# Kernel tuning notes

Hardware: AMD Instinct MI355X
Metric: run time of the kernel (lower is better)

The kernel has to match this reference:

```python
import jax, jax.numpy as jnp
import numpy as np

FRACTAL_OUTPUT = (5, 5)            # (a, b); requires 5 * num_kernels == a*b
PERC_THRESHOLD = 0.59275
NEXT_SHAPE = (224, 224)
K_END = int(0.4 * FRACTAL_OUTPUT[0] * FRACTAL_OUTPUT[1] + 1)   # 11
KERNEL_SIZES = list(range(3, K_END + 1, 2))                    # [3,5,7,9,11]


def setup_inputs() -> dict:
    key = jax.random.key(0)
    inputs = jax.random.uniform(key, (64, 224, 224, 3), dtype=jnp.float32) * 255.0
    return {"inputs": inputs}


def _extract_patches(x, k):
    # tf.image.extract_patches(sizes=strides=k, SAME) == zero-pad + space-to-depth
    B, H, W, C = x.shape
    rows, cols = -(-H // k), -(-W // k)
    ph, pw = rows * k - H, cols * k - W
    x = jnp.pad(x, ((0, 0), (ph // 2, ph - ph // 2), (pw // 2, pw - pw // 2), (0, 0)))
    x = x.reshape(B, rows, k, cols, k, C).transpose(0, 1, 3, 2, 4, 5)
    return x.reshape(B * rows * cols, k, k, C), rows * cols


def _binarize(patches, k, ch):
    # distance function: 1 iff |channel value - center pixel channel value| <= k
    center = patches[:, k // 2, k // 2, ch][:, None, None]
    return (jnp.abs(patches[..., ch] - center) <= k).astype(jnp.int32)


def _connected_stats(binp, k):
    # 4-connected components via min-label propagation (== tfa connected_components
    # up to relabeling; we only need #components and max label count incl. background)
    N = binp.shape[0]
    idx = jnp.arange(1, k * k + 1, dtype=jnp.int32).reshape(k, k)
    INF = jnp.int32(k * k + 2)
    lbl0 = jnp.where(binp > 0, idx, 0)

    def step(_, lbl):
        v = jnp.where(binp > 0, lbl, INF)
        pad = lambda a, w: jnp.pad(a, ((0, 0),) + w, constant_values=INF)
        up    = pad(v, ((1, 0), (0, 0)))[:, :-1, :]
        down  = pad(v, ((0, 1), (0, 0)))[:, 1:, :]
        left  = pad(v, ((0, 0), (1, 0)))[:, :, :-1]
        right = pad(v, ((0, 0), (0, 1)))[:, :, 1:]
        m = jnp.minimum(jnp.minimum(v, up), jnp.minimum(jnp.minimum(down, left), right))
        return jnp.where(binp > 0, m, 0)

    lbl = jax.lax.fori_loop(0, k * k, step, lbl0)  # k*k iters guarantee convergence
    ncomp = jnp.sum((binp > 0) & (lbl == idx), axis=(1, 2)).astype(jnp.int32)
    lblf = lbl.reshape(N, k * k)
    cnt = jnp.zeros((N, k * k + 1), jnp.int32).at[jnp.arange(N)[:, None], lblf].add(1)
    return ncomp, cnt.max(axis=1)  # (#components, most-common label count incl bg 0)


def _components(inputs, k, ch):
    B = inputs.shape[0]
    patches, P = _extract_patches(inputs, k)
    binp = _binarize(patches, k, ch)                    # (B*P, k, k)
    ones = binp.sum(axis=(1, 2)).reshape(B, P)          # int counts per patch
    # tf.bincount(minlength=1, maxlength=k*k): bins 0..k*k-1, value k*k dropped
    cnt = jnp.zeros((B, k * k + 1), jnp.float32).at[jnp.arange(B)[:, None], ones].add(1.0)
    prob = cnt[:, : k * k] / P                          # (B, k*k)
    n = jnp.arange(1, k * k + 1, dtype=jnp.float32)
    fd = (prob / n).sum(1)
    m = (prob * n).sum(1)
    m2 = ((prob * prob) * n).sum(1)
    lac = (m2 - m * m) / (m * m)
    perc = ((ones.astype(jnp.float32) / (k * k)) >= PERC_THRESHOLD).astype(jnp.int32)
    acp = perc.sum(1) // P                              # tf integer reduce_mean
    ncomp, marea = _connected_stats(binp, k)
    acn = ncomp.reshape(B, P).sum(1) // P
    acma = marea.reshape(B, P).sum(1) // P
    return jnp.stack([acn.astype(jnp.float32), acp.astype(jnp.float32),
                      acma.astype(jnp.float32), lac, fd], axis=1)   # (B, 5)


def _rearrange(c):
    # group metric-major: all acn over kernels, then acp, acma, lac, fd
    return jnp.concatenate([c[:, mm::5] for mm in range(5)], axis=1)


def reference(inputs):
    B = inputs.shape[0]
    chans = []
    for ch in range(3):
        comps = jnp.concatenate([_components(inputs, k, ch) for k in KERNEL_SIZES], axis=1)
        chans.append(_rearrange(comps).reshape(B, FRACTAL_OUTPUT[0], FRACTAL_OUTPUT[1]))
    out = jnp.stack(chans, axis=3)                      # (B, a, b, 3)
    return jax.image.resize(out, (B, NEXT_SHAPE[0], NEXT_SHAPE[1], 3), method='bilinear')
```

## Files before the change

kernel.cpp:

```cpp
#include <hip/hip_runtime.h>

#define HW 224
#define NIMG 64
#define NPIX ((size_t)NIMG * HW * HW)
#define NSLICE 8
#define ACC_STRIDE 128
#define NCOMBO (NIMG * 15)
#define ACC_BYTES (NCOMBO * ACC_STRIDE * 4)

typedef unsigned long long u64;

struct U128 { u64 lo, hi; };

__device__ __forceinline__ u64  u_or  (u64 a, u64 b){ return a | b; }
__device__ __forceinline__ u64  u_and (u64 a, u64 b){ return a & b; }
__device__ __forceinline__ u64  u_andn(u64 a, u64 b){ return a & ~b; }
__device__ __forceinline__ bool u_eq(u64 a, u64 b){ return a == b; }
__device__ __forceinline__ bool u_nz(u64 a){ return a != 0ull; }
__device__ __forceinline__ u64  u_shl(u64 a, int n){ return a << n; }
__device__ __forceinline__ u64  u_shr(u64 a, int n){ return a >> n; }
__device__ __forceinline__ int  u_pop(u64 a){ return __popcll(a); }
__device__ __forceinline__ u64  u_low(u64 a){ return a & (0ull - a); }

__device__ __forceinline__ U128 u_or  (U128 a, U128 b){ return {a.lo|b.lo, a.hi|b.hi}; }
__device__ __forceinline__ U128 u_and (U128 a, U128 b){ return {a.lo&b.lo, a.hi&b.hi}; }
__device__ __forceinline__ U128 u_andn(U128 a, U128 b){ return {a.lo&~b.lo, a.hi&~b.hi}; }
__device__ __forceinline__ bool u_eq(U128 a, U128 b){ return a.lo==b.lo && a.hi==b.hi; }
__device__ __forceinline__ bool u_nz(U128 a){ return (a.lo | a.hi) != 0ull; }
__device__ __forceinline__ U128 u_shl(U128 a, int n){
    return { a.lo << n, (a.hi << n) | (a.lo >> (64 - n)) };
}
__device__ __forceinline__ U128 u_shr(U128 a, int n){
    return { (a.lo >> n) | (a.hi << (64 - n)), a.hi >> n };
}
__device__ __forceinline__ int u_pop(U128 a){ return __popcll(a.lo) + __popcll(a.hi); }
__device__ __forceinline__ U128 u_low(U128 a){
    if (a.lo) return { a.lo & (0ull - a.lo), 0ull };
    return { 0ull, a.hi & (0ull - a.hi) };
}

template<bool B, class T, class F> struct sel        { using type = T; };
template<class T, class F>         struct sel<false, T, F> { using type = F; };

template<int K>
__device__ __forceinline__ void load_row(const float* __restrict__ p, float* r) {
#pragma unroll
    for (int j = 0; j + 4 <= K; j += 4) {
        float4 v; __builtin_memcpy(&v, p + j, 16);
        r[j] = v.x; r[j + 1] = v.y; r[j + 2] = v.z; r[j + 3] = v.w;
    }
    if constexpr ((K & 3) >= 2) {
        constexpr int b = (K / 4) * 4;
        float2 v; __builtin_memcpy(&v, p + b, 8);
        r[b] = v.x; r[b + 1] = v.y;
    }
    if constexpr (K & 1) r[K - 1] = p[K - 1];
}

template<int K, int S, class M>
__device__ __forceinline__ void do_patch(const float* __restrict__ img, int p,
                                         M leftCol, M rightCol,
                                         int* bins, int& t_perc, int& t_ncomp,
                                         int& t_marea) {
    constexpr int KK   = K * K;
    constexpr int ROWS = (HW + K - 1) / K;
    constexpr int PAD  = (ROWS * K - HW) / 2;

    const int pr = p / ROWS, pc = p - pr * ROWS;
    const int y0 = pr * K - PAD, x0 = pc * K - PAD;

    M msk;
    if constexpr (KK <= 64) msk = 0ull; else msk = U128{0, 0};

    const bool fast = (S == 1) && (y0 >= 0) && (x0 >= 0) &&
                      (y0 + K <= HW) && (x0 + K <= HW);
    if (fast) {
        if constexpr (K <= 9) {
            float r[K][K];
#pragma unroll
            for (int i = 0; i < K; i++)
                load_row<K>(img + (size_t)(y0 + i) * HW + x0, r[i]);
            const float cen = r[K / 2][K / 2];
#pragma unroll
            for (int i = 0; i < K; i++) {
#pragma unroll
                for (int j = 0; j < K; j++) {
                    const u64 bit = (fabsf(r[i][j] - cen) <= (float)K) ? 1ull : 0ull;
                    const int cb = i * K + j;
                    if constexpr (KK <= 64) msk |= bit << cb;
                    else { if (cb < 64) msk.lo |= bit << cb; else msk.hi |= bit << (cb - 64); }
                }
            }
        } else {
            const float cen = img[(size_t)(y0 + K / 2) * HW + (x0 + K / 2)];
#pragma unroll
            for (int i = 0; i < K; i++) {
                float r[K];
                load_row<K>(img + (size_t)(y0 + i) * HW + x0, r);
#pragma unroll
                for (int j = 0; j < K; j++) {
                    const u64 bit = (fabsf(r[j] - cen) <= (float)K) ? 1ull : 0ull;
                    const int cb = i * K + j;
                    if constexpr (KK <= 64) msk |= bit << cb;
                    else { if (cb < 64) msk.lo |= bit << cb; else msk.hi |= bit << (cb - 64); }
                }
            }
        }
    } else {
        const float cen = img[((size_t)(y0 + K / 2) * HW + (x0 + K / 2)) * S];
#pragma unroll
        for (int i = 0; i < K; i++) {
            const int y = y0 + i;
            const bool yin = (unsigned)y < (unsigned)HW;
#pragma unroll
            for (int j = 0; j < K; j++) {
                const int x = x0 + j;
                const bool inb = yin && ((unsigned)x < (unsigned)HW);
                const float v = inb ? img[((size_t)y * HW + x) * S] : 0.0f;
                const u64 bit = (fabsf(v - cen) <= (float)K) ? 1ull : 0ull;
                const int cb = i * K + j;
                if constexpr (KK <= 64) msk |= bit << cb;
                else { if (cb < 64) msk.lo |= bit << cb; else msk.hi |= bit << (cb - 64); }
            }
        }
    }
    const int ones = u_pop(msk);

    M nbm = u_or(u_or(u_shl(u_andn(msk, rightCol), 1),
                      u_shr(u_andn(msk, leftCol ), 1)),
                 u_or(u_shl(msk, K), u_shr(msk, K)));
    M iso = u_andn(msk, nbm);
    const int niso = u_pop(iso);
    int ncomp = niso, maxsz = (niso > 0) ? 1 : 0;
    M m = u_andn(msk, iso);
    while (u_nz(m)) {
        M s = u_low(m);
        for (;;) {
            M g = u_or(s, u_or(u_or(u_shl(u_andn(s, rightCol), 1),
                                    u_shr(u_andn(s, leftCol ), 1)),
                               u_or(u_shl(s, K), u_shr(s, K))));
            g = u_and(g, m);
            if (u_eq(g, s)) break;
            s = g;
        }
        ncomp++;
        const int sz = u_pop(s);
        if (sz > maxsz) maxsz = sz;
        m = u_andn(m, s);
    }

    const int bgcnt = KK - ones;
    const int marea = (bgcnt > maxsz) ? bgcnt : maxsz;
    t_ncomp += ncomp;
    t_marea += marea;
    if ((float)ones / (float)KK >= 0.59275f) t_perc++;
    atomicAdd(&bins[ones], 1);
}

template<int K>
__device__ __forceinline__ void make_colmasks(u64& lcl, u64& lch, u64& rcl, u64& rch) {
    lcl = lch = rcl = rch = 0;
#pragma unroll
    for (int i = 0; i < K; i++) {
        const int cl = i * K, cr = i * K + K - 1;
        if (cl < 64) lcl |= 1ull << cl; else lch |= 1ull << (cl - 64);
        if (cr < 64) rcl |= 1ull << cr; else rch |= 1ull << (cr - 64);
    }
}

template<int K, int S>
__device__ __forceinline__ void job_body(const float* __restrict__ img,
                                         int slice, int lane, int* hist,
                                         int* __restrict__ gout) {
    constexpr int ROWS = (HW + K - 1) / K;
    constexpr int P    = ROWS * ROWS;
    constexpr int KK   = K * K;
    using M = typename sel<(KK <= 64), u64, U128>::type;

    u64 lcl, lch, rcl, rch;
    make_colmasks<K>(lcl, lch, rcl, rch);
    M leftCol, rightCol;
    if constexpr (KK <= 64) { leftCol = lcl; rightCol = rcl; }
    else { leftCol = U128{lcl, lch}; rightCol = U128{rcl, rch}; }

    for (int s = lane; s <= KK; s += 64) hist[s] = 0;

    const int pstart = (slice * P) / NSLICE;
    const int pend   = ((slice + 1) * P) / NSLICE;

    int t_perc = 0, t_ncomp = 0, t_marea = 0;
    if constexpr (K <= 5) {
#pragma unroll 2
        for (int p = pstart + lane; p < pend; p += 64)
            do_patch<K, S, M>(img, p, leftCol, rightCol, hist,
                              t_perc, t_ncomp, t_marea);
    } else {
        for (int p = pstart + lane; p < pend; p += 64)
            do_patch<K, S, M>(img, p, leftCol, rightCol, hist,
                              t_perc, t_ncomp, t_marea);
    }

#pragma unroll
    for (int off = 32; off; off >>= 1) {
        t_perc  += __shfl_down(t_perc,  off);
        t_ncomp += __shfl_down(t_ncomp, off);
        t_marea += __shfl_down(t_marea, off);
    }
    if (lane == 0) {
        atomicAdd(&gout[124], t_perc);
        atomicAdd(&gout[125], t_ncomp);
        atomicAdd(&gout[126], t_marea);
    }
    for (int s = lane; s <= KK; s += 64) {
        const int v = hist[s];
        if (v) atomicAdd(&gout[s], v);
    }
}

template<int S>
__global__ __launch_bounds__(64) void fractal_stats(const float* __restrict__ in,
                                                    int* __restrict__ gacc) {
    const int B     = blockIdx.x;
    const int x     = B & 7;
    const int j     = B >> 3;
    const int gl    = j / 40;
    const int inner = j - gl * 40;
    const int g     = gl * 8 + x;
    const int b     = g / 3, ch = g - b * 3;
    const int kidx  = inner >> 3;
    const int slice = inner & 7;

    __shared__ int hist[124];

    const float* img = (S == 1) ? in + ((size_t)ch * NIMG + b) * HW * HW
                                : in + (size_t)b * HW * HW * 3 + ch;
    int* gout = gacc + (g * 5 + kidx) * ACC_STRIDE;

    switch (kidx) {
        case 0: job_body<3,  S>(img, slice, threadIdx.x, hist, gout); break;
        case 1: job_body<5,  S>(img, slice, threadIdx.x, hist, gout); break;
        case 2: job_body<7,  S>(img, slice, threadIdx.x, hist, gout); break;
        case 3: job_body<9,  S>(img, slice, threadIdx.x, hist, gout); break;
        case 4: job_body<11, S>(img, slice, threadIdx.x, hist, gout); break;
    }
}

__global__ __launch_bounds__(256) void fractal_resize_acc(const int* __restrict__ gacc,
                                                          float* __restrict__ out,
                                                          int total) {
    const int q = blockIdx.x, b = blockIdx.y;
    __shared__ float vals[75];

    if (threadIdx.x < 15) {
        const int rem  = threadIdx.x;
        const int ch   = rem / 5;
        const int kidx = rem % 5;
        const int K    = 3 + 2 * kidx;
        const int ROWS = (HW + K - 1) / K;
        const int P    = ROWS * ROWS;
        const int KK   = K * K;

        const int* a = gacc + (b * 15 + rem) * ACC_STRIDE;
        const float Pf = (float)P;
        float fd = 0.0f, m1 = 0.0f, m2 = 0.0f;
        for (int s = 0; s < KK; s++) {
            const float prob = (float)a[s] / Pf;
            const float n = (float)(s + 1);
            fd += prob / n;
            m1 += prob * n;
            m2 += prob * prob * n;
        }
        const float lac = (m2 - m1 * m1) / (m1 * m1);
        vals[(0 * 5 + kidx) * 3 + ch] = (float)(a[125] / P);
        vals[(1 * 5 + kidx) * 3 + ch] = (float)(a[124] / P);
        vals[(2 * 5 + kidx) * 3 + ch] = (float)(a[126] / P);
        vals[(3 * 5 + kidx) * 3 + ch] = lac;
        vals[(4 * 5 + kidx) * 3 + ch] = fd;
    }
    __syncthreads();

    const int x = threadIdx.x;
    if (x >= HW) return;

    const float sc = 5.0f / 224.0f;
    const float ux = ((float)x + 0.5f) * sc - 0.5f;
    const float fx = floorf(ux);
    const float wx = ux - fx;
    int x0 = (int)fx, x1 = x0 + 1;
    if (x0 < 0) x0 = 0; if (x1 > 4) x1 = 4;

    for (int y = q * 56; y < q * 56 + 56; ++y) {
        const float uy = ((float)y + 0.5f) * sc - 0.5f;
        const float fy = floorf(uy);
        const float wy = uy - fy;
        int y0 = (int)fy, y1 = y0 + 1;
        if (y0 < 0) y0 = 0; if (y1 > 4) y1 = 4;

        const float w00 = (1.0f - wy) * (1.0f - wx), w01 = (1.0f - wy) * wx;
        const float w10 = wy * (1.0f - wx),          w11 = wy * wx;

        const int base = ((b * HW + y) * HW + x) * 3;
        if (base + 3 > total) continue;
#pragma unroll
        for (int ch = 0; ch < 3; ch++) {
            out[base + ch] = w00 * vals[(y0 * 5 + x0) * 3 + ch]
                           + w01 * vals[(y0 * 5 + x1) * 3 + ch]
                           + w10 * vals[(y1 * 5 + x0) * 3 + ch]
                           + w11 * vals[(y1 * 5 + x1) * 3 + ch];
        }
    }
}

template<int K, int S>
__device__ __forceinline__ void stats_body_full(const float* __restrict__ img,
                                                float* __restrict__ o,
                                                int hist4[4][124], int* sums) {
    constexpr int KK   = K * K;
    constexpr int ROWS = (HW + K - 1) / K;
    constexpr int P    = ROWS * ROWS;
    using M = typename sel<(KK <= 64), u64, U128>::type;
    const int wid = threadIdx.x >> 6;

    u64 lcl, lch, rcl, rch;
    make_colmasks<K>(lcl, lch, rcl, rch);
    M leftCol, rightCol;
    if constexpr (KK <= 64) { leftCol = lcl; rightCol = rcl; }
    else { leftCol = U128{lcl, lch}; rightCol = U128{rcl, rch}; }

    int t_perc = 0, t_ncomp = 0, t_marea = 0;
    for (int p = threadIdx.x; p < P; p += 256)
        do_patch<K, S, M>(img, p, leftCol, rightCol, hist4[wid],
                          t_perc, t_ncomp, t_marea);

    atomicAdd(&sums[0], t_perc);
    atomicAdd(&sums[1], t_ncomp);
    atomicAdd(&sums[2], t_marea);
    __syncthreads();

    if (threadIdx.x == 0) {
        const float Pf = (float)P;
        float fd = 0.0f, m1 = 0.0f, m2 = 0.0f;
        for (int s = 0; s < KK; s++) {
            const float prob = (float)(hist4[0][s] + hist4[1][s] + hist4[2][s] + hist4[3][s]) / Pf;
            const float n = (float)(s + 1);
            fd += prob / n;
            m1 += prob * n;
            m2 += prob * prob * n;
        }
        const float lac = (m2 - m1 * m1) / (m1 * m1);
        o[0]  = (float)(sums[1] / P);
        o[15] = (float)(sums[0] / P);
        o[30] = (float)(sums[2] / P);
        o[45] = lac;
        o[60] = fd;
    }
}

template<int S>
__global__ __launch_bounds__(256) void fractal_stats_full(const float* __restrict__ in,
                                                          float* __restrict__ interm) {
    const int b    = blockIdx.x / 15;
    const int rem  = blockIdx.x % 15;
    const int ch   = rem / 5;
    const int kidx = rem % 5;

    __shared__ int hist[4][124];
    __shared__ int sums[3];
    for (int i = threadIdx.x; i < 4 * 124; i += 256) ((int*)hist)[i] = 0;
    if (threadIdx.x < 3) sums[threadIdx.x] = 0;
    __syncthreads();

    const float* img = in + (size_t)b * HW * HW * 3 + ch;
    float* o = interm + (size_t)b * 75 + kidx * 3 + ch;

    switch (kidx) {
        case 0: stats_body_full<3,  S>(img, o, hist, sums); break;
        case 1: stats_body_full<5,  S>(img, o, hist, sums); break;
        case 2: stats_body_full<7,  S>(img, o, hist, sums); break;
        case 3: stats_body_full<9,  S>(img, o, hist, sums); break;
        case 4: stats_body_full<11, S>(img, o, hist, sums); break;
    }
}

__global__ __launch_bounds__(256) void fractal_resize(const float* __restrict__ interm,
                                                      float* __restrict__ out, int total) {
    const int x = threadIdx.x;
    if (x >= HW) return;
    const int y = blockIdx.x, b = blockIdx.y;

    const float sc = 5.0f / 224.0f;
    const float uy = ((float)y + 0.5f) * sc - 0.5f;
    const float ux = ((float)x + 0.5f) * sc - 0.5f;

    const float fy = floorf(uy), fx = floorf(ux);
    const float wy = uy - fy,    wx = ux - fx;
    int y0 = (int)fy, x0 = (int)fx;
    int y1 = y0 + 1,  x1 = x0 + 1;
    if (y0 < 0) y0 = 0; if (x0 < 0) x0 = 0;
    if (y1 > 4) y1 = 4; if (x1 > 4) x1 = 4;

    const float w00 = (1.0f - wy) * (1.0f - wx), w01 = (1.0f - wy) * wx;
    const float w10 = wy * (1.0f - wx),          w11 = wy * wx;

    const float* gp = interm + (size_t)b * 75;
    const int base = ((b * HW + y) * HW + x) * 3;
    if (base + 3 > total) return;
#pragma unroll
    for (int ch = 0; ch < 3; ch++) {
        out[base + ch] = w00 * gp[(y0 * 5 + x0) * 3 + ch]
                       + w01 * gp[(y0 * 5 + x1) * 3 + ch]
                       + w10 * gp[(y1 * 5 + x0) * 3 + ch]
                       + w11 * gp[(y1 * 5 + x1) * 3 + ch];
    }
}

__global__ __launch_bounds__(256) void deinterleave(const float* __restrict__ in,
                                                    float* __restrict__ planes,
                                                    int* __restrict__ gacc) {
    const int t = blockIdx.x * 256 + threadIdx.x;
    if (t < ACC_BYTES / 16) {
        const int4 z = make_int4(0, 0, 0, 0);
        ((int4*)gacc)[t] = z;
    }
    const size_t pix = (size_t)t * 4;
    if (pix >= NPIX) return;
    float4 a, b, c;
    __builtin_memcpy(&a, in + pix * 3,     16);
    __builtin_memcpy(&b, in + pix * 3 + 4, 16);
    __builtin_memcpy(&c, in + pix * 3 + 8, 16);
    const float4 p0 = make_float4(a.x, a.w, b.z, c.y);
    const float4 p1 = make_float4(a.y, b.x, b.w, c.z);
    const float4 p2 = make_float4(a.z, b.y, c.x, c.w);
    __builtin_memcpy(planes + pix,            &p0, 16);
    __builtin_memcpy(planes + NPIX + pix,     &p1, 16);
    __builtin_memcpy(planes + 2 * NPIX + pix, &p2, 16);
}

extern "C" void kernel_launch(void* const* d_in, const int* in_sizes, int n_in,
                              void* d_out, int out_size, void* d_ws, size_t ws_size,
                              hipStream_t stream) {
    const float* in = (const float*)d_in[0];
    float* out = (float*)d_out;
    float* interm = (float*)d_ws;

    const size_t acc_off    = 19456;
    const size_t planes_off = acc_off + ACC_BYTES;
    const size_t need = planes_off + 3 * NPIX * sizeof(float);

    if (ws_size >= need) {
        int*   gacc   = (int*)((char*)d_ws + acc_off);
        float* planes = (float*)((char*)d_ws + planes_off);
        deinterleave<<<(int)(NPIX / 4 / 256), 256, 0, stream>>>(in, planes, gacc);
        fractal_stats<1><<<192 * 40, 64, 0, stream>>>(planes, gacc);
        fractal_resize_acc<<<dim3(4, NIMG), 256, 0, stream>>>(gacc, out, out_size);
    } else {
        fractal_stats_full<3><<<NIMG * 15, 256, 0, stream>>>(in, interm);
        fractal_resize<<<dim3(HW, NIMG), 256, 0, stream>>>(interm, out, out_size);
    }
}
```

Baseline: 150.8 us.

## Process all three channels per patch from interleaved input, drop deinterleave pass

Removes the separate deinterleave kernel that wrote three channel planes, and instead has each thread read interleaved RGB rows directly and build three binary masks per patch. The per-patch position math and loads are shared across channels. Work is also rebalanced with per-kernel-size slice counts, 109 blocks per image, and the accumulator is zeroed with a memset. In exchange each thread holds more registers and does three connected-component passes, which may lower occupancy and increase divergence.

```diff
diff --git a/kernel.cpp b/kernel.cpp
--- a/kernel.cpp
+++ b/kernel.cpp
@@ -3,7 +3,6 @@
 #define HW 224
 #define NIMG 64
 #define NPIX ((size_t)NIMG * HW * HW)
-#define NSLICE 8
 #define ACC_STRIDE 128
 #define NCOMBO (NIMG * 15)
 #define ACC_BYTES (NCOMBO * ACC_STRIDE * 4)
@@ -39,91 +38,45 @@
     return { 0ull, a.hi & (0ull - a.hi) };
 }
 
+__device__ __forceinline__ void setbit(u64& m, int cb, u64 bit){ m |= bit << cb; }
+__device__ __forceinline__ void setbit(U128& m, int cb, u64 bit){
+    if (cb < 64) m.lo |= bit << cb; else m.hi |= bit << (cb - 64);
+}
+
 template<bool B, class T, class F> struct sel        { using type = T; };
 template<class T, class F>         struct sel<false, T, F> { using type = F; };
 
-template<int K>
-__device__ __forceinline__ void load_row(const float* __restrict__ p, float* r) {
-#pragma unroll
-    for (int j = 0; j + 4 <= K; j += 4) {
+template<int N>
+__device__ __forceinline__ void load_rowN(const float* __restrict__ p, float* r) {
+#pragma unroll
+    for (int j = 0; j + 4 <= N; j += 4) {
         float4 v; __builtin_memcpy(&v, p + j, 16);
         r[j] = v.x; r[j + 1] = v.y; r[j + 2] = v.z; r[j + 3] = v.w;
     }
-    if constexpr ((K & 3) >= 2) {
-        constexpr int b = (K / 4) * 4;
+    if constexpr ((N & 3) >= 2) {
+        constexpr int b = (N / 4) * 4;
         float2 v; __builtin_memcpy(&v, p + b, 8);
         r[b] = v.x; r[b + 1] = v.y;
     }
-    if constexpr (K & 1) r[K - 1] = p[K - 1];
-}
-
-template<int K, int S, class M>
-__device__ __forceinline__ void do_patch(const float* __restrict__ img, int p,
-                                         M leftCol, M rightCol,
-                                         int* bins, int& t_perc, int& t_ncomp,
-                                         int& t_marea) {
-    constexpr int KK   = K * K;
-    constexpr int ROWS = (HW + K - 1) / K;
-    constexpr int PAD  = (ROWS * K - HW) / 2;
-
-    const int pr = p / ROWS, pc = p - pr * ROWS;
-    const int y0 = pr * K - PAD, x0 = pc * K - PAD;
-
-    M msk;
-    if constexpr (KK <= 64) msk = 0ull; else msk = U128{0, 0};
-
-    const bool fast = (S == 1) && (y0 >= 0) && (x0 >= 0) &&
-                      (y0 + K <= HW) && (x0 + K <= HW);
-    if (fast) {
-        if constexpr (K <= 9) {
-            float r[K][K];
-#pragma unroll
-            for (int i = 0; i < K; i++)
-                load_row<K>(img + (size_t)(y0 + i) * HW + x0, r[i]);
-            const float cen = r[K / 2][K / 2];
-#pragma unroll
-            for (int i = 0; i < K; i++) {
-#pragma unroll
-                for (int j = 0; j < K; j++) {
-                    const u64 bit = (fabsf(r[i][j] - cen) <= (float)K) ? 1ull : 0ull;
-                    const int cb = i * K + j;
-                    if constexpr (KK <= 64) msk |= bit << cb;
-                    else { if (cb < 64) msk.lo |= bit << cb; else msk.hi |= bit << (cb - 64); }
-                }
-            }
-        } else {
-            const float cen = img[(size_t)(y0 + K / 2) * HW + (x0 + K / 2)];
-#pragma unroll
-            for (int i = 0; i < K; i++) {
-                float r[K];
-                load_row<K>(img + (size_t)(y0 + i) * HW + x0, r);
-#pragma unroll
-                for (int j = 0; j < K; j++) {
-                    const u64 bit = (fabsf(r[j] - cen) <= (float)K) ? 1ull : 0ull;
-                    const int cb = i * K + j;
-                    if constexpr (KK <= 64) msk |= bit << cb;
-                    else { if (cb < 64) msk.lo |= bit << cb; else msk.hi |= bit << (cb - 64); }
-                }
-            }
-        }
-    } else {
-        const float cen = img[((size_t)(y0 + K / 2) * HW + (x0 + K / 2)) * S];
-#pragma unroll
-        for (int i = 0; i < K; i++) {
-            const int y = y0 + i;
-            const bool yin = (unsigned)y < (unsigned)HW;
-#pragma unroll
-            for (int j = 0; j < K; j++) {
-                const int x = x0 + j;
-                const bool inb = yin && ((unsigned)x < (unsigned)HW);
-                const float v = inb ? img[((size_t)y * HW + x) * S] : 0.0f;
-                const u64 bit = (fabsf(v - cen) <= (float)K) ? 1ull : 0ull;
-                const int cb = i * K + j;
-                if constexpr (KK <= 64) msk |= bit << cb;
-                else { if (cb < 64) msk.lo |= bit << cb; else msk.hi |= bit << (cb - 64); }
-            }
-        }
-    }
+    if constexpr (N & 1) r[N - 1] = p[N - 1];
+}
+
+template<int K>
+__device__ __forceinline__ void make_colmasks(u64& lcl, u64& lch, u64& rcl, u64& rch) {
+    lcl = lch = rcl = rch = 0;
+#pragma unroll
+    for (int i = 0; i < K; i++) {
+        const int cl = i * K, cr = i * K + K - 1;
+        if (cl < 64) lcl |= 1ull << cl; else lch |= 1ull << (cl - 64);
+        if (cr < 64) rcl |= 1ull << cr; else rch |= 1ull << (cr - 64);
+    }
+}
+
+template<int K, class M>
+__device__ __forceinline__ void finish_mask(M msk, M leftCol, M rightCol,
+                                            int* hist, int& t_perc,
+                                            int& t_ncomp, int& t_marea) {
+    constexpr int KK = K * K;
     const int ones = u_pop(msk);
 
     M nbm = u_or(u_or(u_shl(u_andn(msk, rightCol), 1),
@@ -154,27 +107,97 @@
     t_ncomp += ncomp;
     t_marea += marea;
     if ((float)ones / (float)KK >= 0.59275f) t_perc++;
-    atomicAdd(&bins[ones], 1);
+    atomicAdd(&hist[ones], 1);
+}
+
+template<int K, class M>
+__device__ __forceinline__ void do_patch3(const float* __restrict__ img3, int p,
+                                          M leftCol, M rightCol,
+                                          int hist[3][124],
+                                          int* tp, int* tn, int* tm) {
+    constexpr int ROWS = (HW + K - 1) / K;
+    constexpr int PAD  = (ROWS * K - HW) / 2;
+
+    const int pr = p / ROWS, pc = p - pr * ROWS;
+    const int y0 = pr * K - PAD, x0 = pc * K - PAD;
+
+    M m0, m1, m2;
+    if constexpr (sizeof(M) == 8) { m0 = 0ull; m1 = 0ull; m2 = 0ull; }
+    else { m0 = U128{0,0}; m1 = U128{0,0}; m2 = U128{0,0}; }
+
+    const bool fast = (y0 >= 0) && (x0 >= 0) && (y0 + K <= HW) && (x0 + K <= HW);
+    if (fast) {
+        if constexpr (K <= 5) {
+            float t[K][3 * K];
+#pragma unroll
+            for (int i = 0; i < K; i++)
+                load_rowN<3 * K>(img3 + ((size_t)(y0 + i) * HW + x0) * 3, t[i]);
+            const float c0 = t[K / 2][3 * (K / 2) + 0];
+            const float c1 = t[K / 2][3 * (K / 2) + 1];
+            const float c2 = t[K / 2][3 * (K / 2) + 2];
+#pragma unroll
+            for (int i = 0; i < K; i++) {
+#pragma unroll
+                for (int j = 0; j < K; j++) {
+                    const int cb = i * K + j;
+                    setbit(m0, cb, (fabsf(t[i][3*j+0] - c0) <= (float)K) ? 1ull : 0ull);
+                    setbit(m1, cb, (fabsf(t[i][3*j+1] - c1) <= (float)K) ? 1ull : 0ull);
+                    setbit(m2, cb, (fabsf(t[i][3*j+2] - c2) <= (float)K) ? 1ull : 0ull);
+                }
+            }
+        } else {
+            const float* cp = img3 + ((size_t)(y0 + K / 2) * HW + (x0 + K / 2)) * 3;
+            const float c0 = cp[0], c1 = cp[1], c2 = cp[2];
+#pragma unroll
+            for (int i = 0; i < K; i++) {
+                float t[3 * K];
+                load_rowN<3 * K>(img3 + ((size_t)(y0 + i) * HW + x0) * 3, t);
+#pragma unroll
+                for (int j = 0; j < K; j++) {
+                    const int cb = i * K + j;
+                    setbit(m0, cb, (fabsf(t[3*j+0] - c0) <= (float)K) ? 1ull : 0ull);
+                    setbit(m1, cb, (fabsf(t[3*j+1] - c1) <= (float)K) ? 1ull : 0ull);
+                    setbit(m2, cb, (fabsf(t[3*j+2] - c2) <= (float)K) ? 1ull : 0ull);
+                }
+            }
+        }
+    } else {
+        const float* cp = img3 + ((size_t)(y0 + K / 2) * HW + (x0 + K / 2)) * 3;
+        const float c0 = cp[0], c1 = cp[1], c2 = cp[2];
+#pragma unroll
+        for (int i = 0; i < K; i++) {
+            const int y = y0 + i;
+            const bool yin = (unsigned)y < (unsigned)HW;
+#pragma unroll
+            for (int j = 0; j < K; j++) {
+                const int x = x0 + j;
+                const bool inb = yin && ((unsigned)x < (unsigned)HW);
+                const float* q = img3 + ((size_t)y * HW + x) * 3;
+                const float v0 = inb ? q[0] : 0.0f;
+                const float v1 = inb ? q[1] : 0.0f;
+                const float v2 = inb ? q[2] : 0.0f;
+                const int cb = i * K + j;
+                setbit(m0, cb, (fabsf(v0 - c0) <= (float)K) ? 1ull : 0ull);
+                setbit(m1, cb, (fabsf(v1 - c1) <= (float)K) ? 1ull : 0ull);
+                setbit(m2, cb, (fabsf(v2 - c2) <= (float)K) ? 1ull : 0ull);
+            }
+        }
+    }
+
+    finish_mask<K, M>(m0, leftCol, rightCol, hist[0], tp[0], tn[0], tm[0]);
+    finish_mask<K, M>(m1, leftCol, rightCol, hist[1], tp[1], tn[1], tm[1]);
+    finish_mask<K, M>(m2, leftCol, rightCol, hist[2], tp[2], tn[2], tm[2]);
 }
 
 template<int K>
-__device__ __forceinline__ void make_colmasks(u64& lcl, u64& lch, u64& rcl, u64& rch) {
-    lcl = lch = rcl = rch = 0;
-#pragma unroll
-    for (int i = 0; i < K; i++) {
-        const int cl = i * K, cr = i * K + K - 1;
-        if (cl < 64) lcl |= 1ull << cl; else lch |= 1ull << (cl - 64);
-        if (cr < 64) rcl |= 1ull << cr; else rch |= 1ull << (cr - 64);
-    }
-}
-
-template<int K, int S>
-__device__ __forceinline__ void job_body(const float* __restrict__ img,
-                                         int slice, int lane, int* hist,
-                                         int* __restrict__ gout) {
+__device__ __forceinline__ void job_body3(const float* __restrict__ img3,
+                                          int slice, int lane, int hist[3][124],
+                                          int* __restrict__ gout_b, int kidx) {
     constexpr int ROWS = (HW + K - 1) / K;
     constexpr int P    = ROWS * ROWS;
     constexpr int KK   = K * K;
+    constexpr int SLC  = (K == 3) ? 44 : (K == 5) ? 32 : (K == 7) ? 16
+                       : (K == 9) ? 10 : 7;
     using M = typename sel<(KK <= 64), u64, U128>::type;
 
     u64 lcl, lch, rcl, rch;
@@ -183,65 +206,73 @@
     if constexpr (KK <= 64) { leftCol = lcl; rightCol = rcl; }
     else { leftCol = U128{lcl, lch}; rightCol = U128{rcl, rch}; }
 
-    for (int s = lane; s <= KK; s += 64) hist[s] = 0;
-
-    const int pstart = (slice * P) / NSLICE;
-    const int pend   = ((slice + 1) * P) / NSLICE;
-
-    int t_perc = 0, t_ncomp = 0, t_marea = 0;
-    if constexpr (K <= 5) {
-#pragma unroll 2
-        for (int p = pstart + lane; p < pend; p += 64)
-            do_patch<K, S, M>(img, p, leftCol, rightCol, hist,
-                              t_perc, t_ncomp, t_marea);
-    } else {
-        for (int p = pstart + lane; p < pend; p += 64)
-            do_patch<K, S, M>(img, p, leftCol, rightCol, hist,
-                              t_perc, t_ncomp, t_marea);
-    }
+#pragma unroll
+    for (int ch = 0; ch < 3; ch++)
+        for (int s = lane; s <= KK; s += 64) hist[ch][s] = 0;
+
+    const int pstart = (slice * P) / SLC;
+    const int pend   = ((slice + 1) * P) / SLC;
+
+    int tp[3] = {0,0,0}, tn[3] = {0,0,0}, tm[3] = {0,0,0};
+    for (int p = pstart + lane; p < pend; p += 64)
+        do_patch3<K, M>(img3, p, leftCol, rightCol, hist, tp, tn, tm);
 
 #pragma unroll
     for (int off = 32; off; off >>= 1) {
-        t_perc  += __shfl_down(t_perc,  off);
-        t_ncomp += __shfl_down(t_ncomp, off);
-        t_marea += __shfl_down(t_marea, off);
+#pragma unroll
+        for (int ch = 0; ch < 3; ch++) {
+            tp[ch] += __shfl_down(tp[ch], off);
+            tn[ch] += __shfl_down(tn[ch], off);
+            tm[ch] += __shfl_down(tm[ch], off);
+        }
     }
     if (lane == 0) {
-        atomicAdd(&gout[124], t_perc);
-        atomicAdd(&gout[125], t_ncomp);
-        atomicAdd(&gout[126], t_marea);
-    }
-    for (int s = lane; s <= KK; s += 64) {
-        const int v = hist[s];
-        if (v) atomicAdd(&gout[s], v);
-    }
-}
-
-template<int S>
-__global__ __launch_bounds__(64) void fractal_stats(const float* __restrict__ in,
-                                                    int* __restrict__ gacc) {
+#pragma unroll
+        for (int ch = 0; ch < 3; ch++) {
+            int* gout = gout_b + (ch * 5 + kidx) * ACC_STRIDE;
+            atomicAdd(&gout[124], tp[ch]);
+            atomicAdd(&gout[125], tn[ch]);
+            atomicAdd(&gout[126], tm[ch]);
+        }
+    }
+#pragma unroll
+    for (int ch = 0; ch < 3; ch++) {
+        int* gout = gout_b + (ch * 5 + kidx) * ACC_STRIDE;
+        for (int s = lane; s <= KK; s += 64) {
+            const int v = hist[ch][s];
+            if (v) atomicAdd(&gout[s], v);
+        }
+    }
+}
+
+__global__ __launch_bounds__(64) void fractal_stats3(const float* __restrict__ in,
+                                                     int* __restrict__ gacc) {
+    const int lane  = threadIdx.x;
     const int B     = blockIdx.x;
     const int x     = B & 7;
     const int j     = B >> 3;
-    const int gl    = j / 40;
-    const int inner = j - gl * 40;
-    const int g     = gl * 8 + x;
-    const int b     = g / 3, ch = g - b * 3;
-    const int kidx  = inner >> 3;
-    const int slice = inner & 7;
-
-    __shared__ int hist[124];
-
-    const float* img = (S == 1) ? in + ((size_t)ch * NIMG + b) * HW * HW
-                                : in + (size_t)b * HW * HW * 3 + ch;
-    int* gout = gacc + (g * 5 + kidx) * ACC_STRIDE;
+    const int gl    = j / 109;
+    const int inner = j - gl * 109;
+    const int b     = gl * 8 + x;
+
+    __shared__ int hist[3][124];
+
+    int kidx, slice;
+    if      (inner < 7)  { kidx = 4; slice = inner;      }
+    else if (inner < 17) { kidx = 3; slice = inner - 7;  }
+    else if (inner < 33) { kidx = 2; slice = inner - 17; }
+    else if (inner < 77) { kidx = 0; slice = inner - 33; }
+    else                 { kidx = 1; slice = inner - 77; }
+
+    const float* img3 = in + (size_t)b * HW * HW * 3;
+    int* gout_b = gacc + (size_t)b * 15 * ACC_STRIDE;
 
     switch (kidx) {
-        case 0: job_body<3,  S>(img, slice, threadIdx.x, hist, gout); break;
-        case 1: job_body<5,  S>(img, slice, threadIdx.x, hist, gout); break;
-        case 2: job_body<7,  S>(img, slice, threadIdx.x, hist, gout); break;
-        case 3: job_body<9,  S>(img, slice, threadIdx.x, hist, gout); break;
-        case 4: job_body<11, S>(img, slice, threadIdx.x, hist, gout); break;
+        case 0: job_body3<3 >(img3, slice, lane, hist, gout_b, 0); break;
+        case 1: job_body3<5 >(img3, slice, lane, hist, gout_b, 1); break;
+        case 2: job_body3<7 >(img3, slice, lane, hist, gout_b, 2); break;
+        case 3: job_body3<9 >(img3, slice, lane, hist, gout_b, 3); break;
+        case 4: job_body3<11>(img3, slice, lane, hist, gout_b, 4); break;
     }
 }
 
@@ -311,13 +342,14 @@
     }
 }
 
-template<int K, int S>
-__device__ __forceinline__ void stats_body_full(const float* __restrict__ img,
+template<int K>
+__device__ __forceinline__ void stats_body_full(const float* __restrict__ img3,
                                                 float* __restrict__ o,
                                                 int hist4[4][124], int* sums) {
     constexpr int KK   = K * K;
     constexpr int ROWS = (HW + K - 1) / K;
     constexpr int P    = ROWS * ROWS;
+    constexpr int PAD  = (ROWS * K - HW) / 2;
     using M = typename sel<(KK <= 64), u64, U128>::type;
     const int wid = threadIdx.x >> 6;
 
@@ -328,9 +360,27 @@
     else { leftCol = U128{lcl, lch}; rightCol = U128{rcl, rch}; }
 
     int t_perc = 0, t_ncomp = 0, t_marea = 0;
-    for (int p = threadIdx.x; p < P; p += 256)
-        do_patch<K, S, M>(img, p, leftCol, rightCol, hist4[wid],
+    for (int p = threadIdx.x; p < P; p += 256) {
+        const int pr = p / ROWS, pc = p - pr * ROWS;
+        const int y0 = pr * K - PAD, x0 = pc * K - PAD;
+        const float cen = img3[((size_t)(y0 + K / 2) * HW + (x0 + K / 2)) * 3];
+        M msk;
+        if constexpr (KK <= 64) msk = 0ull; else msk = U128{0, 0};
+#pragma unroll
+        for (int i = 0; i < K; i++) {
+            const int y = y0 + i;
+            const bool yin = (unsigned)y < (unsigned)HW;
+#pragma unroll
+            for (int j = 0; j < K; j++) {
+                const int x = x0 + j;
+                const bool inb = yin && ((unsigned)x < (unsigned)HW);
+                const float v = inb ? img3[((size_t)y * HW + x) * 3] : 0.0f;
+                setbit(msk, i * K + j, (fabsf(v - cen) <= (float)K) ? 1ull : 0ull);
+            }
+        }
+        finish_mask<K, M>(msk, leftCol, rightCol, hist4[wid],
                           t_perc, t_ncomp, t_marea);
+    }
 
     atomicAdd(&sums[0], t_perc);
     atomicAdd(&sums[1], t_ncomp);
@@ -356,7 +406,6 @@
     }
 }
 
-template<int S>
 __global__ __launch_bounds__(256) void fractal_stats_full(const float* __restrict__ in,
                                                           float* __restrict__ interm) {
     const int b    = blockIdx.x / 15;
@@ -370,15 +419,15 @@
     if (threadIdx.x < 3) sums[threadIdx.x] = 0;
     __syncthreads();
 
-    const float* img = in + (size_t)b * HW * HW * 3 + ch;
+    const float* img3 = in + (size_t)b * HW * HW * 3 + ch;
     float* o = interm + (size_t)b * 75 + kidx * 3 + ch;
 
     switch (kidx) {
-        case 0: stats_body_full<3,  S>(img, o, hist, sums); break;
-        case 1: stats_body_full<5,  S>(img, o, hist, sums); break;
-        case 2: stats_body_full<7,  S>(img, o, hist, sums); break;
-        case 3: stats_body_full<9,  S>(img, o, hist, sums); break;
-        case 4: stats_body_full<11, S>(img, o, hist, sums); break;
+        case 0: stats_body_full<3 >(img3, o, hist, sums); break;
+        case 1: stats_body_full<5 >(img3, o, hist, sums); break;
+        case 2: stats_body_full<7 >(img3, o, hist, sums); break;
+        case 3: stats_body_full<9 >(img3, o, hist, sums); break;
+        case 4: stats_body_full<11>(img3, o, hist, sums); break;
     }
 }
 
@@ -414,28 +463,6 @@
     }
 }
 
-__global__ __launch_bounds__(256) void deinterleave(const float* __restrict__ in,
-                                                    float* __restrict__ planes,
-                                                    int* __restrict__ gacc) {
-    const int t = blockIdx.x * 256 + threadIdx.x;
-    if (t < ACC_BYTES / 16) {
-        const int4 z = make_int4(0, 0, 0, 0);
-        ((int4*)gacc)[t] = z;
-    }
-    const size_t pix = (size_t)t * 4;
-    if (pix >= NPIX) return;
-    float4 a, b, c;
-    __builtin_memcpy(&a, in + pix * 3,     16);
-    __builtin_memcpy(&b, in + pix * 3 + 4, 16);
-    __builtin_memcpy(&c, in + pix * 3 + 8, 16);
-    const float4 p0 = make_float4(a.x, a.w, b.z, c.y);
-    const float4 p1 = make_float4(a.y, b.x, b.w, c.z);
-    const float4 p2 = make_float4(a.z, b.y, c.x, c.w);
-    __builtin_memcpy(planes + pix,            &p0, 16);
-    __builtin_memcpy(planes + NPIX + pix,     &p1, 16);
-    __builtin_memcpy(planes + 2 * NPIX + pix, &p2, 16);
-}
-
 extern "C" void kernel_launch(void* const* d_in, const int* in_sizes, int n_in,
                               void* d_out, int out_size, void* d_ws, size_t ws_size,
                               hipStream_t stream) {
@@ -443,18 +470,16 @@
     float* out = (float*)d_out;
     float* interm = (float*)d_ws;
 
-    const size_t acc_off    = 19456;
-    const size_t planes_off = acc_off + ACC_BYTES;
-    const size_t need = planes_off + 3 * NPIX * sizeof(float);
+    const size_t acc_off = 19456;
+    const size_t need    = acc_off + ACC_BYTES;
 
     if (ws_size >= need) {
-        int*   gacc   = (int*)((char*)d_ws + acc_off);
-        float* planes = (float*)((char*)d_ws + planes_off);
-        deinterleave<<<(int)(NPIX / 4 / 256), 256, 0, stream>>>(in, planes, gacc);
-        fractal_stats<1><<<192 * 40, 64, 0, stream>>>(planes, gacc);
+        int* gacc = (int*)((char*)d_ws + acc_off);
+        hipMemsetAsync(gacc, 0, ACC_BYTES, stream);
+        fractal_stats3<<<64 * 109, 64, 0, stream>>>(in, gacc);
         fractal_resize_acc<<<dim3(4, NIMG), 256, 0, stream>>>(gacc, out, out_size);
     } else {
-        fractal_stats_full<3><<<NIMG * 15, 256, 0, stream>>>(in, interm);
+        fractal_stats_full<<<NIMG * 15, 256, 0, stream>>>(in, interm);
         fractal_resize<<<dim3(HW, NIMG), 256, 0, stream>>>(interm, out, out_size);
     }
 }
```

New measurement: 181.8 us. 1.21x slower.
